# Optimization experiments

Measured on AMD Instinct MI355X. Metric: run time of the kernel, lower is better.

The kernel has to match this reference:

```python
import jax, jax.numpy as jnp
import numpy as np
import math

B, T, D, H = 64, 256, 512, 1024


def setup_inputs() -> dict:
    key = jax.random.key(0)
    ks = jax.random.split(key, 11)
    stdv = 1.0 / math.sqrt(H)

    def u(k, shape):
        return jax.random.uniform(k, shape, jnp.float32, -stdv, stdv)

    return {
        "x": jax.random.normal(ks[0], (B, T, D), jnp.float32),
        "h0": jax.random.normal(ks[1], (B, H), jnp.float32),
        "ctx": jax.random.normal(ks[2], (B, H), jnp.float32),
        "Wi": u(ks[3], (3 * H, D)), "bi": u(ks[4], (3 * H,)),
        "Wh": u(ks[5], (2 * H, H)), "bh": u(ks[6], (2 * H,)),
        "Wp": u(ks[7], (3 * H, H)), "bp": u(ks[8], (3 * H,)),
        "Wc": u(ks[9], (H, H)),     "bc": u(ks[10], (H,)),
    }


def reference(x, h0, ctx, Wi, bi, Wh, bh, Wp, bp, Wc, bc):
    # Input gates for all timesteps in one batched GEMM: [B,T,3H] -> time-major [T,B,3H]
    ig_all = jnp.einsum("btd,gd->tbg", x, Wi) + bi
    # Peephole gate depends only on ctx -> compute once. [B,3H]
    p_r, p_i, p_n = jnp.split(ctx @ Wp.T + bp, 3, axis=-1)

    def step(h, ig):
        i_r, i_i, i_n = jnp.split(ig, 3, axis=-1)
        h_r, h_i = jnp.split(h @ Wh.T + bh, 2, axis=-1)
        resetgate = jax.nn.sigmoid(i_r + h_r + p_r)
        inputgate = jax.nn.sigmoid(i_i + h_i + p_i)
        h_n = (resetgate * h) @ Wc.T + bc
        newgate = jnp.tanh(i_n + h_n + p_n)
        hy = h + inputgate * (newgate - h)
        return hy, hy

    hT, ys = jax.lax.scan(step, h0, ig_all)  # ys: [T,B,H]
    output = jnp.transpose(ys, (1, 0, 2))    # [B,T,H]
    return output, hT
```

## Files before the change

### kernel.cpp

```cpp
#include <hip/hip_runtime.h>
#include <hip/hip_bf16.h>
#include <math.h>

#define Bz 64
#define Tz 256
#define Dz 512
#define Hz 1024
#define G3 3072
#define NBK 64

typedef short bf16x8 __attribute__((ext_vector_type(8)));
typedef float f32x4 __attribute__((ext_vector_type(4)));

__device__ __forceinline__ float sigm(float x){ return 1.0f/(1.0f+expf(-x)); }

__device__ __forceinline__ unsigned short f2b(float f){
  union{float f;unsigned u;}v; v.f=f;
  unsigned r = v.u + 0x7FFFu + ((v.u>>16)&1u);
  return (unsigned short)(r>>16);
}
__device__ __forceinline__ float b2f(unsigned short s){
  union{unsigned u;float f;}v; v.u = ((unsigned)s)<<16; return v.f;
}
__device__ __forceinline__ unsigned pk2(float a, float b){
  return (unsigned)f2b(a) | ((unsigned)f2b(b)<<16);
}

__device__ __forceinline__ unsigned long long cld64(const void* p){
  return __hip_atomic_load((const unsigned long long*)p, __ATOMIC_RELAXED, __HIP_MEMORY_SCOPE_AGENT);
}
__device__ __forceinline__ void cst64(void* p, unsigned long long v){
  __hip_atomic_store((unsigned long long*)p, v, __ATOMIC_RELAXED, __HIP_MEMORY_SCOPE_AGENT);
}
__device__ __forceinline__ float2 cldf2(const float* p){
  union { unsigned long long u; float2 f; } U; U.u = cld64(p); return U.f;
}
__device__ __forceinline__ void cstf2(float* p, float a, float b){
  union { unsigned long long u; float2 f; } U; U.f = make_float2(a,b); cst64(p, U.u);
}
__device__ __forceinline__ int cld32(const int* p){
  return __hip_atomic_load(p, __ATOMIC_RELAXED, __HIP_MEMORY_SCOPE_AGENT);
}
__device__ __forceinline__ void cst32(int* p, int v){
  __hip_atomic_store(p, v, __ATOMIC_RELAXED, __HIP_MEMORY_SCOPE_AGENT);
}
__device__ __forceinline__ void waitcan(const int* can, int tgt){
  int l = threadIdx.x & 63;
  while (!__all(cld32(can + l) >= tgt))
    __builtin_amdgcn_s_sleep(1);
  asm volatile("" ::: "memory");
}

#define KCHUNK 128
#define LDA 132
template<int COLS, int KDIM>
__device__ __forceinline__ void gemm_core(const float* __restrict__ Abase, int rowStride,
                                          const float* __restrict__ W,
                                          int jc0, int b, int tid,
                                          float* __restrict__ acc, float* __restrict__ lds)
{
#pragma unroll
  for (int c=0;c<COLS;c++) acc[c]=0.0f;
  constexpr int C4 = KCHUNK/4;
  for (int kb=0; kb<KDIM; kb+=KCHUNK) {
    __syncthreads();
    for (int i = tid; i < Bz*C4; i += 256) {
      int r  = i / C4;
      int c4 = i % C4;
      float4 v = *(const float4*)(Abase + (size_t)r*rowStride + kb + c4*4);
      *(float4*)(lds + r*LDA + c4*4) = v;
    }
    __syncthreads();
    const float* arow  = lds + b*LDA;
    const float* wbase = W + (size_t)jc0*KDIM + kb;
    for (int k=0;k<KCHUNK;k+=4) {
      float4 a = *(const float4*)(arow + k);
#pragma unroll
      for (int c=0;c<COLS;c++) {
        float4 w = *(const float4*)(wbase + (size_t)c*KDIM + k);
        acc[c] = fmaf(a.x,w.x,fmaf(a.y,w.y,fmaf(a.z,w.z,fmaf(a.w,w.w,acc[c]))));
      }
    }
  }
}

__global__ __launch_bounds__(256)
void kP(const float* __restrict__ ctx, const float* __restrict__ Wp,
        const float* __restrict__ bp, const float* __restrict__ bh,
        const float* __restrict__ bc, const float* __restrict__ bi,
        float* __restrict__ pT)
{
  __shared__ float lds[Bz*LDA];
  int tid=threadIdx.x; int b=tid&63;
  int wv=__builtin_amdgcn_readfirstlane(tid>>6);
  int jc0 = blockIdx.x*16 + wv*4;
  float acc[4];
  gemm_core<4, Hz>(ctx, Hz, Wp, jc0, b, tid, acc, lds);
#pragma unroll
  for(int c=0;c<4;c++){
    int j=jc0+c;
    float v = acc[c] + bp[j] + bi[j] + (j < 2*Hz ? bh[j] : bc[j-2*Hz]);
    pT[(size_t)j*64 + b] = v;
  }
}

__global__ __launch_bounds__(256)
void kI(const float* __restrict__ h0, float* __restrict__ hF, unsigned short* __restrict__ hB)
{
  int b = blockIdx.x;
  int j = threadIdx.x*4;
  float4 v = *(const float4*)(h0 + (size_t)b*Hz + j);
  *(float4*)(hF + ((size_t)(j>>2)*64 + b)*4) = v;
  unsigned long long pk = (unsigned long long)pk2(v.x,v.y)
                        | ((unsigned long long)pk2(v.z,v.w) << 32);
  *(unsigned long long*)(hB + (size_t)b*Hz + j) = pk;
}

__global__ __launch_bounds__(1024)
void kAm(const float* __restrict__ x, const float* __restrict__ Wi,
         const float* __restrict__ pT, unsigned short* __restrict__ igT)
{
  __shared__ unsigned short wiF[4*16*64*8];
  __shared__ unsigned short xs[64*528];
  __shared__ unsigned short igs[64*64];
  const int tid = threadIdx.x;
  const int lane = tid & 63;
  const int w = __builtin_amdgcn_readfirstlane(tid >> 6);
  const int j0 = blockIdx.x * 64;
  const int t0 = blockIdx.y * 16;
  const int mt = w >> 2, nt = w & 3;
  const int bb = nt*16 + (lane & 15);
  const int q  = lane >> 4;
  const int jl = mt*16 + q*4;

  for (int idx = tid; idx < 4096; idx += 1024) {
    int mt2 = idx >> 10;
    int ks = (idx >> 6) & 15;
    int ln = idx & 63;
    int j = j0 + mt2*16 + (ln & 15);
    int k = ks*32 + (ln >> 4)*8;
    const float* s = Wi + (size_t)j*Dz + k;
    unsigned short* d = wiF + (size_t)idx*8;
#pragma unroll
    for (int qq=0;qq<8;qq++) d[qq] = f2b(s[qq]);
  }
  float pv[4];
#pragma unroll
  for (int r=0;r<4;r++) pv[r] = pT[(size_t)(j0+jl+r)*64 + bb];

  for (int it=0; it<16; it++) {
    int t = t0 + it;
    __syncthreads();
    for (int i = tid; i < 64*32; i += 1024) {
      int b = i >> 5, c = i & 31;
      const float* s = x + ((size_t)b*Tz + t)*Dz + c*16;
      unsigned* d = (unsigned*)(xs + (size_t)b*528 + c*16);
      float4 v0 = *(const float4*)(s);
      float4 v1 = *(const float4*)(s+4);
      float4 v2 = *(const float4*)(s+8);
      float4 v3 = *(const float4*)(s+12);
      d[0]=pk2(v0.x,v0.y); d[1]=pk2(v0.z,v0.w);
      d[2]=pk2(v1.x,v1.y); d[3]=pk2(v1.z,v1.w);
      d[4]=pk2(v2.x,v2.y); d[5]=pk2(v2.z,v2.w);
      d[6]=pk2(v3.x,v3.y); d[7]=pk2(v3.z,v3.w);
    }
    __syncthreads();
    f32x4 acc = {0.f,0.f,0.f,0.f};
    const unsigned short* bsrc = xs + (size_t)bb*528 + q*8;
#pragma unroll
    for (int ks=0; ks<16; ks++) {
      bf16x8 a = *(const bf16x8*)(wiF + ((size_t)(mt*16+ks)*64 + lane)*8);
      bf16x8 b = *(const bf16x8*)(bsrc + ks*32);
      acc = __builtin_amdgcn_mfma_f32_16x16x32_bf16(a, b, acc, 0, 0, 0);
    }
#pragma unroll
    for (int r=0;r<4;r++) igs[(size_t)(jl+r)*64 + bb] = f2b(acc[r] + pv[r]);
    __syncthreads();
    if (tid < 512) {
      int j = tid >> 3, seg = tid & 7;
      *(uint4*)(igT + ((size_t)t*G3 + j0 + j)*64 + seg*8) =
        *(const uint4*)(igs + (size_t)j*64 + seg*8);
    }
  }
}

__global__ __launch_bounds__(1024)
void krec(const float* __restrict__ Wh, const float* __restrict__ Wc,
          const unsigned short* __restrict__ igT,
          float* __restrict__ hF0, float* __restrict__ hF1,
          unsigned short* __restrict__ hB0, unsigned short* __restrict__ hB1,
          unsigned short* __restrict__ rhB, float* __restrict__ iT,
          float* __restrict__ out, int* canP, int* canH)
{
  __shared__ unsigned short whF[2*32*64*8];
  __shared__ unsigned short wcF[32*64*8];
  __shared__ float red[16*64*4];
  const int tid = threadIdx.x;
  const int lane = tid & 63;
  const int w = __builtin_amdgcn_readfirstlane(tid >> 6);
  const int n = blockIdx.x;

  for (int idx = tid; idx < 4096; idx += 1024) {
    int mt = idx >> 11;
    int ks = (idx >> 6) & 31;
    int ln = idx & 63;
    int j = n*32 + mt*16 + (ln & 15);
    int k = ks*32 + (ln >> 4)*8;
    const float* s = Wh + (size_t)j*Hz + k;
    unsigned short* d = whF + (size_t)idx*8;
#pragma unroll
    for (int qq=0;qq<8;qq++) d[qq] = f2b(s[qq]);
  }
  for (int idx = tid; idx < 2048; idx += 1024) {
    int ks = (idx >> 6) & 31;
    int ln = idx & 63;
    int j = n*16 + (ln & 15);
    int k = ks*32 + (ln >> 4)*8;
    const float* s = Wc + (size_t)j*Hz + k;
    unsigned short* d = wcF + (size_t)idx*8;
#pragma unroll
    for (int qq=0;qq<8;qq++) d[qq] = f2b(s[qq]);
  }

  for (int t=0;t<Tz;t++) {
    const unsigned short* igt = igT + (size_t)t*G3*64;
    const unsigned short* hBr = (t&1) ? hB1 : hB0;
    unsigned short*       hBw = (t&1) ? hB0 : hB1;
    const float*          hFr = (t&1) ? hF1 : hF0;
    float*                hFw = (t&1) ? hF0 : hF1;
    {
      int tp = w & 7, kh = w >> 3;
      int mt = tp >> 2, nt = tp & 3;
      int bb = nt*16 + (lane & 15);
      int q  = lane >> 4;
      int jg = n*32 + mt*16 + q*4;
      float igv[4], hv[4];
      if (w < 8) {
#pragma unroll
        for (int r=0;r<4;r++) igv[r] = b2f(igt[(size_t)(jg+r)*64 + bb]);
      }
      if (w == 0) waitcan(canH, t);
      __syncthreads();
      if (w < 8 && n < 32) {
        const float* hp = hFr + ((size_t)(jg>>2)*64 + bb)*4;
        float2 a01 = cldf2(hp), a23 = cldf2(hp+2);
        hv[0]=a01.x; hv[1]=a01.y; hv[2]=a23.x; hv[3]=a23.y;
      }
      bf16x8 bfr[16];
      {
        unsigned voff = (unsigned)(bb*2048 + q*16 + kh*1024);
        asm volatile(
          "global_load_dwordx4 %0, %16, %17 sc0 sc1\n\t"
          "global_load_dwordx4 %1, %16, %17 offset:64 sc0 sc1\n\t"
          "global_load_dwordx4 %2, %16, %17 offset:128 sc0 sc1\n\t"
          "global_load_dwordx4 %3, %16, %17 offset:192 sc0 sc1\n\t"
          "global_load_dwordx4 %4, %16, %17 offset:256 sc0 sc1\n\t"
          "global_load_dwordx4 %5, %16, %17 offset:320 sc0 sc1\n\t"
          "global_load_dwordx4 %6, %16, %17 offset:384 sc0 sc1\n\t"
          "global_load_dwordx4 %7, %16, %17 offset:448 sc0 sc1\n\t"
          "global_load_dwordx4 %8, %16, %17 offset:512 sc0 sc1\n\t"
          "global_load_dwordx4 %9, %16, %17 offset:576 sc0 sc1\n\t"
          "global_load_dwordx4 %10, %16, %17 offset:640 sc0 sc1\n\t"
          "global_load_dwordx4 %11, %16, %17 offset:704 sc0 sc1\n\t"
          "global_load_dwordx4 %12, %16, %17 offset:768 sc0 sc1\n\t"
          "global_load_dwordx4 %13, %16, %17 offset:832 sc0 sc1\n\t"
          "global_load_dwordx4 %14, %16, %17 offset:896 sc0 sc1\n\t"
          "global_load_dwordx4 %15, %16, %17 offset:960 sc0 sc1\n\t"
          "s_waitcnt vmcnt(0)"
          : "=v"(bfr[0]), "=v"(bfr[1]), "=v"(bfr[2]), "=v"(bfr[3]),
            "=v"(bfr[4]), "=v"(bfr[5]), "=v"(bfr[6]), "=v"(bfr[7]),
            "=v"(bfr[8]), "=v"(bfr[9]), "=v"(bfr[10]), "=v"(bfr[11]),
            "=v"(bfr[12]), "=v"(bfr[13]), "=v"(bfr[14]), "=v"(bfr[15])
          : "v"(voff), "s"(hBr)
          : "memory");
      }
      f32x4 acc = {0.f,0.f,0.f,0.f};
      const unsigned short* asrc = whF + ((size_t)(mt*32 + kh*16)*64 + lane)*8;
#pragma unroll
      for (int ks=0; ks<16; ks++) {
        bf16x8 a = *(const bf16x8*)(asrc + (size_t)ks*64*8);
        acc = __builtin_amdgcn_mfma_f32_16x16x32_bf16(a, bfr[ks], acc, 0, 0, 0);
      }
      *(f32x4*)(red + ((size_t)w*64 + lane)*4) = acc;
      __syncthreads();
      if (w < 8) {
        f32x4 o  = *(const f32x4*)(red + ((size_t)w*64+lane)*4);
        f32x4 p2 = *(const f32x4*)(red + ((size_t)(w+8)*64+lane)*4);
        if (n < 32) {
          unsigned long long pk = 0;
#pragma unroll
          for (int r=0;r<4;r++) {
            float g = sigm(o[r] + p2[r] + igv[r]);
            pk |= (unsigned long long)f2b(g * hv[r]) << (16*r);
          }
          cst64(rhB + (size_t)bb*Hz + jg, pk);
        } else {
          float g0 = sigm(o[0] + p2[0] + igv[0]);
          float g1 = sigm(o[1] + p2[1] + igv[1]);
          float g2 = sigm(o[2] + p2[2] + igv[2]);
          float g3 = sigm(o[3] + p2[3] + igv[3]);
          float* ip = iT + ((size_t)((jg-1024)>>2)*64 + bb)*4;
          cstf2(ip, g0, g1); cstf2(ip+2, g2, g3);
        }
      }
      __syncthreads();
      if (tid == 0) cst32(canP + n, t+1);
    }
    {
      int nt = w & 3, kq = w >> 2;
      int bb = nt*16 + (lane & 15);
      int q  = lane >> 4;
      int jn = n*16 + q*4;
      float igv[4], hv[4], iv[4];
      if (w < 4) {
#pragma unroll
        for (int r=0;r<4;r++) igv[r] = b2f(igt[(size_t)(2048+jn+r)*64 + bb]);
      }
      if (w == 0) waitcan(canP, t+1);
      __syncthreads();
      if (w < 4) {
        const float* hp = hFr + ((size_t)(jn>>2)*64 + bb)*4;
        float2 a01 = cldf2(hp), a23 = cldf2(hp+2);
        hv[0]=a01.x; hv[1]=a01.y; hv[2]=a23.x; hv[3]=a23.y;
        const float* ip = iT + ((size_t)(jn>>2)*64 + bb)*4;
        float2 b01 = cldf2(ip), b23 = cldf2(ip+2);
        iv[0]=b01.x; iv[1]=b01.y; iv[2]=b23.x; iv[3]=b23.y;
      }
      bf16x8 bfr[8];
      {
        unsigned voff = (unsigned)(bb*2048 + q*16 + kq*512);
        asm volatile(
          "global_load_dwordx4 %0, %8, %9 sc0 sc1\n\t"
          "global_load_dwordx4 %1, %8, %9 offset:64 sc0 sc1\n\t"
          "global_load_dwordx4 %2, %8, %9 offset:128 sc0 sc1\n\t"
          "global_load_dwordx4 %3, %8, %9 offset:192 sc0 sc1\n\t"
          "global_load_dwordx4 %4, %8, %9 offset:256 sc0 sc1\n\t"
          "global_load_dwordx4 %5, %8, %9 offset:320 sc0 sc1\n\t"
          "global_load_dwordx4 %6, %8, %9 offset:384 sc0 sc1\n\t"
          "global_load_dwordx4 %7, %8, %9 offset:448 sc0 sc1\n\t"
          "s_waitcnt vmcnt(0)"
          : "=v"(bfr[0]), "=v"(bfr[1]), "=v"(bfr[2]), "=v"(bfr[3]),
            "=v"(bfr[4]), "=v"(bfr[5]), "=v"(bfr[6]), "=v"(bfr[7])
          : "v"(voff), "s"(rhB)
          : "memory");
      }
      f32x4 acc = {0.f,0.f,0.f,0.f};
#pragma unroll
      for (int ks=0; ks<8; ks++) {
        bf16x8 a = *(const bf16x8*)(wcF + ((size_t)(kq*8+ks)*64 + lane)*8);
        acc = __builtin_amdgcn_mfma_f32_16x16x32_bf16(a, bfr[ks], acc, 0, 0, 0);
      }
      *(f32x4*)(red + ((size_t)w*64 + lane)*4) = acc;
      __syncthreads();
      if (w < 4) {
        f32x4 s0 = *(const f32x4*)(red + ((size_t)w*64+lane)*4);
        f32x4 s1 = *(const f32x4*)(red + ((size_t)(w+4)*64+lane)*4);
        f32x4 s2 = *(const f32x4*)(red + ((size_t)(w+8)*64+lane)*4);
        f32x4 s3 = *(const f32x4*)(red + ((size_t)(w+12)*64+lane)*4);
        float hy4[4];
        unsigned long long pk = 0;
#pragma unroll
        for (int r=0;r<4;r++) {
          float g  = s0[r]+s1[r]+s2[r]+s3[r] + igv[r];
          float ng = tanhf(g);
          float hy = hv[r] + iv[r]*(ng - hv[r]);
          hy4[r] = hy;
          pk |= (unsigned long long)f2b(hy) << (16*r);
        }
        float* hp = hFw + ((size_t)(jn>>2)*64 + bb)*4;
        cstf2(hp,   hy4[0], hy4[1]);
        cstf2(hp+2, hy4[2], hy4[3]);
        cst64(hBw + (size_t)bb*Hz + jn, pk);
        float4 ov; ov.x=hy4[0]; ov.y=hy4[1]; ov.z=hy4[2]; ov.w=hy4[3];
        *(float4*)(out + ((size_t)bb*Tz + t)*Hz + jn) = ov;
      }
      __syncthreads();
      if (tid == 0) cst32(canH + n, t+1);
    }
  }
}

__global__ __launch_bounds__(256)
void ktr(const float* __restrict__ hF, float* __restrict__ hN)
{
  int b = blockIdx.x;
  int j = threadIdx.x*4;
  float4 v = *(const float4*)(hF + ((size_t)(j>>2)*64 + b)*4);
  *(float4*)(hN + (size_t)b*Hz + j) = v;
}

extern "C" void kernel_launch(void* const* d_in, const int* in_sizes, int n_in,
                              void* d_out, int out_size, void* d_ws, size_t ws_size,
                              hipStream_t stream)
{
  const float* x   = (const float*)d_in[0];
  const float* h0  = (const float*)d_in[1];
  const float* ctx = (const float*)d_in[2];
  const float* Wi  = (const float*)d_in[3];
  const float* bi  = (const float*)d_in[4];
  const float* Wh  = (const float*)d_in[5];
  const float* bh  = (const float*)d_in[6];
  const float* Wp  = (const float*)d_in[7];
  const float* bp  = (const float*)d_in[8];
  const float* Wc  = (const float*)d_in[9];
  const float* bc  = (const float*)d_in[10];
  float* out = (float*)d_out;

  char* wsp = (char*)d_ws;
  float* pT  = (float*)wsp; wsp += (size_t)G3*64*sizeof(float);
  float* hF0 = (float*)wsp; wsp += (size_t)Hz*64*sizeof(float);
  float* hF1 = (float*)wsp; wsp += (size_t)Hz*64*sizeof(float);
  float* iT  = (float*)wsp; wsp += (size_t)Hz*64*sizeof(float);
  unsigned short* hB0 = (unsigned short*)wsp; wsp += (size_t)Bz*Hz*2;
  unsigned short* hB1 = (unsigned short*)wsp; wsp += (size_t)Bz*Hz*2;
  unsigned short* rhB = (unsigned short*)wsp; wsp += (size_t)Bz*Hz*2;
  int* canP = (int*)wsp; wsp += 512;
  int* canH = canP + 64;
  unsigned short* igT = (unsigned short*)wsp;

  hipMemsetAsync(canP, 0, 512, stream);
  kP  <<<dim3(G3/16),   256,  0, stream>>>(ctx, Wp, bp, bh, bc, bi, pT);
  kI  <<<dim3(64),      256,  0, stream>>>(h0, hF0, hB0);
  kAm <<<dim3(48,16),   1024, 0, stream>>>(x, Wi, pT, igT);
  krec<<<dim3(NBK),     1024, 0, stream>>>(Wh, Wc, igT, hF0, hF1, hB0, hB1, rhB, iT, out, canP, canH);
  ktr <<<dim3(64),      256,  0, stream>>>(hF0, out + (size_t)Bz*Tz*Hz);
}
```

Before: 4.823 ms.

## Replace block-wide flag waits with per-wave fine-grained dependency waits

Each wave now polls only the producer-block flags for the K-slice it consumes (canH for its 16 producers, canP for its 8 plus the matching input-gate block), instead of wave 0 polling all 64 flags and then a block barrier. The gate GEMM is re-tiled so each wave handles one batch tile and both M tiles over a quarter of K, which reuses the B fragment and halves per-wave global loads, at the cost of a four-way LDS reduction. Loads of the previous hidden state and the input gate move after the reduction. The intent is to let waves start as soon as their own dependencies are ready and to shorten the serial critical path per timestep, at the cost of more polling traffic across waves.

Result: faster. 3.972 ms (-17.6%).

```diff
diff --git a/kernel.cpp b/kernel.cpp
--- a/kernel.cpp
+++ b/kernel.cpp
@@ -43,12 +43,6 @@
 }
 __device__ __forceinline__ void cst32(int* p, int v){
   __hip_atomic_store(p, v, __ATOMIC_RELAXED, __HIP_MEMORY_SCOPE_AGENT);
-}
-__device__ __forceinline__ void waitcan(const int* can, int tgt){
-  int l = threadIdx.x & 63;
-  while (!__all(cld32(can + l) >= tgt))
-    __builtin_amdgcn_s_sleep(1);
-  asm volatile("" ::: "memory");
 }
 
 #define KCHUNK 128
@@ -194,7 +188,7 @@
 {
   __shared__ unsigned short whF[2*32*64*8];
   __shared__ unsigned short wcF[32*64*8];
-  __shared__ float red[16*64*4];
+  __shared__ float red[32*64*4];
   const int tid = threadIdx.x;
   const int lane = tid & 63;
   const int w = __builtin_amdgcn_readfirstlane(tid >> 6);
@@ -222,6 +216,11 @@
     for (int qq=0;qq<8;qq++) d[qq] = f2b(s[qq]);
   }
 
+  const int nt = w & 3;
+  const int kh = w >> 2;
+  const int bb = nt*16 + (lane & 15);
+  const int q  = lane >> 4;
+
   for (int t=0;t<Tz;t++) {
     const unsigned short* igt = igT + (size_t)t*G3*64;
     const unsigned short* hBr = (t&1) ? hB1 : hB0;
@@ -229,76 +228,73 @@
     const float*          hFr = (t&1) ? hF1 : hF0;
     float*                hFw = (t&1) ? hF0 : hF1;
     {
-      int tp = w & 7, kh = w >> 3;
-      int mt = tp >> 2, nt = tp & 3;
-      int bb = nt*16 + (lane & 15);
-      int q  = lane >> 4;
-      int jg = n*32 + mt*16 + q*4;
-      float igv[4], hv[4];
+      float igv[4];
       if (w < 8) {
+        int jg = n*32 + (w>>2)*16 + q*4;
 #pragma unroll
         for (int r=0;r<4;r++) igv[r] = b2f(igt[(size_t)(jg+r)*64 + bb]);
       }
-      if (w == 0) waitcan(canH, t);
-      __syncthreads();
-      if (w < 8 && n < 32) {
-        const float* hp = hFr + ((size_t)(jg>>2)*64 + bb)*4;
-        float2 a01 = cldf2(hp), a23 = cldf2(hp+2);
-        hv[0]=a01.x; hv[1]=a01.y; hv[2]=a23.x; hv[3]=a23.y;
-      }
-      bf16x8 bfr[16];
       {
-        unsigned voff = (unsigned)(bb*2048 + q*16 + kh*1024);
+        const int* p = canH + kh*16 + (lane & 15);
+        while (!__all(cld32(p) >= t)) __builtin_amdgcn_s_sleep(2);
+        asm volatile("" ::: "memory");
+      }
+      bf16x8 bfr[8];
+      {
+        unsigned voff = (unsigned)(bb*2048 + q*16 + kh*512);
         asm volatile(
-          "global_load_dwordx4 %0, %16, %17 sc0 sc1\n\t"
-          "global_load_dwordx4 %1, %16, %17 offset:64 sc0 sc1\n\t"
-          "global_load_dwordx4 %2, %16, %17 offset:128 sc0 sc1\n\t"
-          "global_load_dwordx4 %3, %16, %17 offset:192 sc0 sc1\n\t"
-          "global_load_dwordx4 %4, %16, %17 offset:256 sc0 sc1\n\t"
-          "global_load_dwordx4 %5, %16, %17 offset:320 sc0 sc1\n\t"
-          "global_load_dwordx4 %6, %16, %17 offset:384 sc0 sc1\n\t"
-          "global_load_dwordx4 %7, %16, %17 offset:448 sc0 sc1\n\t"
-          "global_load_dwordx4 %8, %16, %17 offset:512 sc0 sc1\n\t"
-          "global_load_dwordx4 %9, %16, %17 offset:576 sc0 sc1\n\t"
-          "global_load_dwordx4 %10, %16, %17 offset:640 sc0 sc1\n\t"
-          "global_load_dwordx4 %11, %16, %17 offset:704 sc0 sc1\n\t"
-          "global_load_dwordx4 %12, %16, %17 offset:768 sc0 sc1\n\t"
-          "global_load_dwordx4 %13, %16, %17 offset:832 sc0 sc1\n\t"
-          "global_load_dwordx4 %14, %16, %17 offset:896 sc0 sc1\n\t"
-          "global_load_dwordx4 %15, %16, %17 offset:960 sc0 sc1\n\t"
+          "global_load_dwordx4 %0, %8, %9 sc0 sc1\n\t"
+          "global_load_dwordx4 %1, %8, %9 offset:64 sc0 sc1\n\t"
+          "global_load_dwordx4 %2, %8, %9 offset:128 sc0 sc1\n\t"
+          "global_load_dwordx4 %3, %8, %9 offset:192 sc0 sc1\n\t"
+          "global_load_dwordx4 %4, %8, %9 offset:256 sc0 sc1\n\t"
+          "global_load_dwordx4 %5, %8, %9 offset:320 sc0 sc1\n\t"
+          "global_load_dwordx4 %6, %8, %9 offset:384 sc0 sc1\n\t"
+          "global_load_dwordx4 %7, %8, %9 offset:448 sc0 sc1\n\t"
           "s_waitcnt vmcnt(0)"
           : "=v"(bfr[0]), "=v"(bfr[1]), "=v"(bfr[2]), "=v"(bfr[3]),
-            "=v"(bfr[4]), "=v"(bfr[5]), "=v"(bfr[6]), "=v"(bfr[7]),
-            "=v"(bfr[8]), "=v"(bfr[9]), "=v"(bfr[10]), "=v"(bfr[11]),
-            "=v"(bfr[12]), "=v"(bfr[13]), "=v"(bfr[14]), "=v"(bfr[15])
+            "=v"(bfr[4]), "=v"(bfr[5]), "=v"(bfr[6]), "=v"(bfr[7])
           : "v"(voff), "s"(hBr)
           : "memory");
       }
-      f32x4 acc = {0.f,0.f,0.f,0.f};
-      const unsigned short* asrc = whF + ((size_t)(mt*32 + kh*16)*64 + lane)*8;
-#pragma unroll
-      for (int ks=0; ks<16; ks++) {
-        bf16x8 a = *(const bf16x8*)(asrc + (size_t)ks*64*8);
-        acc = __builtin_amdgcn_mfma_f32_16x16x32_bf16(a, bfr[ks], acc, 0, 0, 0);
-      }
-      *(f32x4*)(red + ((size_t)w*64 + lane)*4) = acc;
+      f32x4 acc0 = {0.f,0.f,0.f,0.f}, acc1 = {0.f,0.f,0.f,0.f};
+      const unsigned short* a0 = whF + ((size_t)(kh*8)*64 + lane)*8;
+      const unsigned short* a1 = whF + ((size_t)(32 + kh*8)*64 + lane)*8;
+#pragma unroll
+      for (int ks=0; ks<8; ks++) {
+        bf16x8 A0 = *(const bf16x8*)(a0 + (size_t)ks*512);
+        bf16x8 A1 = *(const bf16x8*)(a1 + (size_t)ks*512);
+        acc0 = __builtin_amdgcn_mfma_f32_16x16x32_bf16(A0, bfr[ks], acc0, 0, 0, 0);
+        acc1 = __builtin_amdgcn_mfma_f32_16x16x32_bf16(A1, bfr[ks], acc1, 0, 0, 0);
+      }
+      *(f32x4*)(red + ((size_t)((kh*4+nt)*2+0)*64 + lane)*4) = acc0;
+      *(f32x4*)(red + ((size_t)((kh*4+nt)*2+1)*64 + lane)*4) = acc1;
       __syncthreads();
       if (w < 8) {
-        f32x4 o  = *(const f32x4*)(red + ((size_t)w*64+lane)*4);
-        f32x4 p2 = *(const f32x4*)(red + ((size_t)(w+8)*64+lane)*4);
+        int emt = w >> 2, ent = w & 3;
+        int jg = n*32 + emt*16 + q*4;
+        f32x4 s = {0.f,0.f,0.f,0.f};
+#pragma unroll
+        for (int kk=0; kk<4; kk++) {
+          f32x4 v = *(const f32x4*)(red + ((size_t)((kk*4+ent)*2+emt)*64 + lane)*4);
+          s[0]+=v[0]; s[1]+=v[1]; s[2]+=v[2]; s[3]+=v[3];
+        }
         if (n < 32) {
+          const float* hp = hFr + ((size_t)(jg>>2)*64 + bb)*4;
+          float2 a01 = cldf2(hp), a23 = cldf2(hp+2);
+          float hv[4] = {a01.x, a01.y, a23.x, a23.y};
           unsigned long long pk = 0;
 #pragma unroll
           for (int r=0;r<4;r++) {
-            float g = sigm(o[r] + p2[r] + igv[r]);
+            float g = sigm(s[r] + igv[r]);
             pk |= (unsigned long long)f2b(g * hv[r]) << (16*r);
           }
           cst64(rhB + (size_t)bb*Hz + jg, pk);
         } else {
-          float g0 = sigm(o[0] + p2[0] + igv[0]);
-          float g1 = sigm(o[1] + p2[1] + igv[1]);
-          float g2 = sigm(o[2] + p2[2] + igv[2]);
-          float g3 = sigm(o[3] + p2[3] + igv[3]);
+          float g0 = sigm(s[0] + igv[0]);
+          float g1 = sigm(s[1] + igv[1]);
+          float g2 = sigm(s[2] + igv[2]);
+          float g3 = sigm(s[3] + igv[3]);
           float* ip = iT + ((size_t)((jg-1024)>>2)*64 + bb)*4;
           cstf2(ip, g0, g1); cstf2(ip+2, g2, g3);
         }
@@ -307,28 +303,22 @@
       if (tid == 0) cst32(canP + n, t+1);
     }
     {
-      int nt = w & 3, kq = w >> 2;
-      int bb = nt*16 + (lane & 15);
-      int q  = lane >> 4;
-      int jn = n*16 + q*4;
-      float igv[4], hv[4], iv[4];
+      float igv[4];
       if (w < 4) {
+        int jn = n*16 + q*4;
 #pragma unroll
         for (int r=0;r<4;r++) igv[r] = b2f(igt[(size_t)(2048+jn+r)*64 + bb]);
       }
-      if (w == 0) waitcan(canP, t+1);
-      __syncthreads();
-      if (w < 4) {
-        const float* hp = hFr + ((size_t)(jn>>2)*64 + bb)*4;
-        float2 a01 = cldf2(hp), a23 = cldf2(hp+2);
-        hv[0]=a01.x; hv[1]=a01.y; hv[2]=a23.x; hv[3]=a23.y;
-        const float* ip = iT + ((size_t)(jn>>2)*64 + bb)*4;
-        float2 b01 = cldf2(ip), b23 = cldf2(ip+2);
-        iv[0]=b01.x; iv[1]=b01.y; iv[2]=b23.x; iv[3]=b23.y;
+      {
+        int pi = kh*8 + (lane & 7);
+        if (w == 0 && lane >= 56) pi = 32 + (n >> 1);
+        const int* p = canP + pi;
+        while (!__all(cld32(p) >= t+1)) __builtin_amdgcn_s_sleep(2);
+        asm volatile("" ::: "memory");
       }
       bf16x8 bfr[8];
       {
-        unsigned voff = (unsigned)(bb*2048 + q*16 + kq*512);
+        unsigned voff = (unsigned)(bb*2048 + q*16 + kh*512);
         asm volatile(
           "global_load_dwordx4 %0, %8, %9 sc0 sc1\n\t"
           "global_load_dwordx4 %1, %8, %9 offset:64 sc0 sc1\n\t"
@@ -347,7 +337,7 @@
       f32x4 acc = {0.f,0.f,0.f,0.f};
 #pragma unroll
       for (int ks=0; ks<8; ks++) {
-        bf16x8 a = *(const bf16x8*)(wcF + ((size_t)(kq*8+ks)*64 + lane)*8);
+        bf16x8 a = *(const bf16x8*)(wcF + ((size_t)(kh*8+ks)*64 + lane)*8);
         acc = __builtin_amdgcn_mfma_f32_16x16x32_bf16(a, bfr[ks], acc, 0, 0, 0);
       }
       *(f32x4*)(red + ((size_t)w*64 + lane)*4) = acc;
@@ -357,6 +347,13 @@
         f32x4 s1 = *(const f32x4*)(red + ((size_t)(w+4)*64+lane)*4);
         f32x4 s2 = *(const f32x4*)(red + ((size_t)(w+8)*64+lane)*4);
         f32x4 s3 = *(const f32x4*)(red + ((size_t)(w+12)*64+lane)*4);
+        int jn = n*16 + q*4;
+        const float* hp = hFr + ((size_t)(jn>>2)*64 + bb)*4;
+        float2 a01 = cldf2(hp), a23 = cldf2(hp+2);
+        float hv[4] = {a01.x, a01.y, a23.x, a23.y};
+        const float* ip = iT + ((size_t)(jn>>2)*64 + bb)*4;
+        float2 b01 = cldf2(ip), b23 = cldf2(ip+2);
+        float iv[4] = {b01.x, b01.y, b23.x, b23.y};
         float hy4[4];
         unsigned long long pk = 0;
 #pragma unroll
@@ -367,9 +364,9 @@
           hy4[r] = hy;
           pk |= (unsigned long long)f2b(hy) << (16*r);
         }
-        float* hp = hFw + ((size_t)(jn>>2)*64 + bb)*4;
-        cstf2(hp,   hy4[0], hy4[1]);
-        cstf2(hp+2, hy4[2], hy4[3]);
+        float* hpw = hFw + ((size_t)(jn>>2)*64 + bb)*4;
+        cstf2(hpw,   hy4[0], hy4[1]);
+        cstf2(hpw+2, hy4[2], hy4[3]);
         cst64(hBw + (size_t)bb*Hz + jn, pk);
         float4 ov; ov.x=hy4[0]; ov.y=hy4[1]; ov.z=hy4[2]; ov.w=hy4[3];
         *(float4*)(out + ((size_t)bb*Tz + t)*Hz + jn) = ov;
```
